# Kernel tuning notes

Hardware: AMD Instinct MI355X
Metric: run time of the kernel (lower is better)

## Reference

```python
import jax, jax.numpy as jnp
import numpy as np

DIM = 2048
HEAD = 256
SEQ = 4096

def setup_inputs() -> dict:
    key = jax.random.key(0)
    ks = jax.random.split(key, 7)
    s = 1.0 / np.sqrt(DIM)
    return {
        "marketStateBatch": jax.random.normal(ks[0], (SEQ, DIM), dtype=jnp.float32),
        "Wq": jax.random.uniform(ks[1], (HEAD, DIM), jnp.float32, -s, s),
        "bq": jax.random.uniform(ks[2], (HEAD,), jnp.float32, -s, s),
        "Wk": jax.random.uniform(ks[3], (HEAD, DIM), jnp.float32, -s, s),
        "bk": jax.random.uniform(ks[4], (HEAD,), jnp.float32, -s, s),
        "Wv": jax.random.uniform(ks[5], (HEAD, DIM), jnp.float32, -s, s),
        "bv": jax.random.uniform(ks[6], (HEAD,), jnp.float32, -s, s),
    }

def reference(marketStateBatch, Wq, bq, Wk, bk, Wv, bv):
    x = marketStateBatch  # [S, D]
    q = x @ Wq.T + bq     # [S, H]
    k = x @ Wk.T + bk     # [S, H]
    v = x @ Wv.T + bv     # [S, H]
    # NOTE: original scales by sqrt(dimensionSize), the INPUT dim, not head dim.
    scores = (q @ k.T) * (1.0 / np.sqrt(DIM))  # [S, S]
    S = x.shape[0]
    causal = jnp.tril(jnp.ones((S, S), dtype=bool))
    scores = jnp.where(causal, scores, -jnp.inf)
    attn = jax.nn.softmax(scores, axis=-1)
    # torch.nan_to_num(attn, 0.0): rows are never all -inf here (diag kept),
    # but replicate the op faithfully.
    attn = jnp.nan_to_num(attn, nan=0.0)
    return attn @ v  # [S, H]
```

## Files before the change

### kernel.cpp

```cpp
#include <hip/hip_runtime.h>
#include <stdint.h>

#define SEQ 4096
#define DIMK 2048
#define HD 256

typedef __attribute__((ext_vector_type(8))) short bf16x8;
typedef __attribute__((ext_vector_type(4))) short u16x4;
typedef __attribute__((ext_vector_type(4))) float f32x4;
typedef unsigned short u16;
typedef unsigned int u32;

#define BAR() asm volatile("s_barrier" ::: "memory")
#define VMCNT(n) asm volatile("s_waitcnt vmcnt(" #n ")" ::: "memory")

__device__ __forceinline__ u16 f2bf(float f) {
    u32 u = __float_as_uint(f);
    u += 0x7FFFu + ((u >> 16) & 1u);
    return (u16)(u >> 16);
}

__device__ __forceinline__ bf16x8 pack8(f32x4 a0, f32x4 a1) {
    bf16x8 v8;
    v8[0]=(short)f2bf(a0[0]); v8[1]=(short)f2bf(a0[1]);
    v8[2]=(short)f2bf(a0[2]); v8[3]=(short)f2bf(a0[3]);
    v8[4]=(short)f2bf(a1[0]); v8[5]=(short)f2bf(a1[1]);
    v8[6]=(short)f2bf(a1[2]); v8[7]=(short)f2bf(a1[3]);
    return v8;
}

__device__ __forceinline__ void gl16(const void* g, void* l) {
    __builtin_amdgcn_global_load_lds(
        (const __attribute__((address_space(1))) void*)g,
        (__attribute__((address_space(3))) void*)l, 16, 0, 0);
}

__global__ __launch_bounds__(256) void cvt_all2(
    const float* __restrict__ x, const float* __restrict__ Wq,
    const float* __restrict__ Wk, const float* __restrict__ Wv,
    u16* __restrict__ xb_sw, u16* __restrict__ wb_sw)
{
    const int y = blockIdx.y;
    int i = blockIdx.x * 256 + threadIdx.x;
    int stride = gridDim.x * 256;
    if (y == 0) {
        for (; i < SEQ*DIMK/8; i += stride) {
            int row = i >> 8, c8 = i & 255;
            f32x4 a0 = *(const f32x4*)(x + (size_t)row*DIMK + c8*8);
            f32x4 a1 = *(const f32x4*)(x + (size_t)row*DIMK + c8*8 + 4);
            int mt = row >> 6, rl = row & 63, kt = c8 >> 3, sl = c8 & 7;
            size_t dst = ((size_t)(mt*32 + kt))*4096 + rl*64 + ((sl ^ (rl&7))*8);
            *(bf16x8*)(xb_sw + dst) = pack8(a0, a1);
        }
    } else {
        const float* W = (y==1) ? Wq : (y==2) ? Wk : Wv;
        for (; i < HD*DIMK/8; i += stride) {
            int row = i >> 8, c8 = i & 255;
            f32x4 a0 = *(const f32x4*)(W + (size_t)row*DIMK + c8*8);
            f32x4 a1 = *(const f32x4*)(W + (size_t)row*DIMK + c8*8 + 4);
            int gr = (y-1)*256 + row;
            int nt = gr >> 7, rl = gr & 127, kt = c8 >> 3, sl = c8 & 7;
            size_t dst = ((size_t)(nt*32 + kt))*8192 + rl*64 + ((sl ^ (rl&7))*8);
            *(bf16x8*)(wb_sw + dst) = pack8(a0, a1);
        }
    }
}

__global__ __launch_bounds__(256) void qkv_gemm2(
    const u16* __restrict__ xb_sw, const u16* __restrict__ wb_sw,
    const float* __restrict__ bq, const float* __restrict__ bk,
    const float* __restrict__ bv,
    u16* __restrict__ qb, u16* __restrict__ kb_t, u16* __restrict__ vt_t)
{
    __shared__ char T[2][24576];

    const int tid = threadIdx.x;
    const int lane = tid & 63;
    const int w = tid >> 6;
    const int r = lane & 15, g = lane >> 4;
    const int wr = w >> 1, wc = w & 1;
    const int mt = blockIdx.x;
    const int y  = blockIdx.y;
    const int z  = y >> 1;
    const float* bias = (z==0) ? bq : (z==1) ? bk : bv;

    const u16* abase = xb_sw + (size_t)mt*32*4096;
    const u16* bbase = wb_sw + (size_t)y*32*8192;

    f32x4 zero = {0.f,0.f,0.f,0.f};
    f32x4 acc[2][4];
    #pragma unroll
    for (int m = 0; m < 2; ++m)
        #pragma unroll
        for (int n = 0; n < 4; ++n) acc[m][n] = zero;

    auto stage = [&](int b, int kt) {
        const u16* ag = abase + (size_t)kt*4096 + w*1024 + lane*8;
        const u16* bg = bbase + (size_t)kt*8192 + w*2048 + lane*8;
        char* al = T[b] + w*2048;
        char* bl = T[b] + 8192 + w*4096;
        gl16(ag,        al);
        gl16(ag + 512,  al + 1024);
        gl16(bg,        bl);
        gl16(bg + 512,  bl + 1024);
        gl16(bg + 1024, bl + 2048);
        gl16(bg + 1536, bl + 3072);
    };

    stage(0, 0);
    stage(1, 1);

    for (int kt = 0; kt < 32; ++kt) {
        if (kt < 31) { VMCNT(6); } else { VMCNT(0); }
        BAR();
        const char* A = T[kt & 1];
        const char* B = T[kt & 1] + 8192;
        #pragma unroll
        for (int kc = 0; kc < 2; ++kc) {
            bf16x8 af[2], bfr[4];
            #pragma unroll
            for (int m = 0; m < 2; ++m) {
                int arow = wr*32 + m*16 + r;
                af[m] = *(const bf16x8*)(A + arow*128 + (((kc*4+g) ^ (arow&7)) << 4));
            }
            #pragma unroll
            for (int n = 0; n < 4; ++n) {
                int brow = wc*64 + n*16 + r;
                bfr[n] = *(const bf16x8*)(B + brow*128 + (((kc*4+g) ^ (brow&7)) << 4));
            }
            #pragma unroll
            for (int m = 0; m < 2; ++m)
                #pragma unroll
                for (int n = 0; n < 4; ++n)
                    acc[m][n] = __builtin_amdgcn_mfma_f32_16x16x32_bf16(
                        af[m], bfr[n], acc[m][n], 0, 0, 0);
        }
        BAR();
        if (kt + 2 < 32) stage(kt & 1, kt + 2);
    }

    const int m0 = mt*64, n0 = y*128;
    const float qs = 0.03187936f;
    if (z == 0) {
        #pragma unroll
        for (int n = 0; n < 4; ++n) {
            int hc = (n0 + wc*64 + n*16 + r) & 255;
            float bcol = bias[hc];
            #pragma unroll
            for (int m = 0; m < 2; ++m) {
                int row0 = m0 + wr*32 + m*16 + g*4;
                #pragma unroll
                for (int j = 0; j < 4; ++j)
                    qb[(size_t)(row0+j)*HD + hc] = f2bf((acc[m][n][j] + bcol) * qs);
            }
        }
    } else if (z == 1) {
        #pragma unroll
        for (int n = 0; n < 4; ++n) {
            int hc = (n0 + wc*64 + n*16 + r) & 255;
            float bcol = bias[hc];
            #pragma unroll
            for (int m = 0; m < 2; ++m) {
                int row0 = m0 + wr*32 + m*16 + g*4;
                #pragma unroll
                for (int j = 0; j < 4; ++j) {
                    int rowj = row0 + j;
                    int t = rowj >> 5, rl = rowj & 31;
                    kb_t[(size_t)t*8192 + rl*256 + (((hc>>3) ^ (rl&7))*8) + (hc&7)]
                        = f2bf(acc[m][n][j] + bcol);
                }
            }
        }
    } else {
        #pragma unroll
        for (int n = 0; n < 4; ++n) {
            int hc = (n0 + wc*64 + n*16 + r) & 255;
            float bcol = bias[hc];
            #pragma unroll
            for (int m = 0; m < 2; ++m) {
                int kv0 = m0 + wr*32 + m*16 + g*4;
                int t = kv0 >> 5, kl = kv0 & 31;
                u16x4 pk;
                #pragma unroll
                for (int j = 0; j < 4; ++j) pk[j] = (short)f2bf(acc[m][n][j] + bcol);
                *(u16x4*)(vt_t + (size_t)t*8192 + hc*32 +
                          (((kl>>3) ^ (hc&3) ^ ((hc>>2)&3))*8) + (kl&7)) = pk;
            }
        }
    }
}

__global__ __launch_bounds__(256) void attn_part3(
    const u16* __restrict__ qb, const u16* __restrict__ kb_t,
    const u16* __restrict__ vt_t,
    float* __restrict__ po, float* __restrict__ pm, float* __restrict__ pl,
    int C32)
{
    __shared__ char Ks[2][16384];
    __shared__ char Vt[2][16384];
    __shared__ char Ps[4][1280];

    const int qt = blockIdx.x;
    const int s  = blockIdx.y;
    const int nt = 2*qt + 2;
    const int ns = (nt + C32 - 1) / C32;
    if (s >= ns) return;
    int pid0 = 0;
    for (int k = 0; k < qt; ++k) pid0 += (2*k + 2 + C32 - 1) / C32;
    const int pid = pid0 + s;
    const int t0 = s * C32;
    const int t1 = min(t0 + C32, nt);

    const int tid = threadIdx.x;
    const int lane = tid & 63;
    const int w = tid >> 6;
    const int r = lane & 15, g = lane >> 4;
    const int qg = qt*64 + w*16 + r;

    bf16x8 qf[8];
    {
        const u16* qp = qb + (size_t)qg*HD + g*8;
        #pragma unroll
        for (int c = 0; c < 8; ++c) qf[c] = *(const bf16x8*)(qp + c*32);
    }
    VMCNT(0);

    auto stage = [&](int b, int t) {
        const u16* kg = kb_t + (size_t)t*8192 + w*2048 + lane*8;
        const u16* vg = vt_t + (size_t)t*8192 + w*2048 + lane*8;
        char* kl = Ks[b] + w*4096;
        char* vl = Vt[b] + w*4096;
        #pragma unroll
        for (int i = 0; i < 4; ++i) gl16(kg + i*512, kl + i*1024);
        #pragma unroll
        for (int i = 0; i < 4; ++i) gl16(vg + i*512, vl + i*1024);
    };

    stage(0, t0);
    if (t0 + 1 < t1) stage(1, t0 + 1);

    f32x4 zero = {0.f,0.f,0.f,0.f};
    f32x4 o[16];
    #pragma unroll
    for (int hf = 0; hf < 16; ++hf) o[hf] = zero;
    float mrun = -__builtin_inff(), lrun = 0.f;
    char* Psw = Ps[w];

    for (int t = t0; t < t1; ++t) {
        if (t + 1 < t1) { VMCNT(8); } else { VMCNT(0); }
        BAR();
        const char* K = Ks[t & 1];
        const char* V = Vt[t & 1];

        f32x4 sv[2];
        __builtin_amdgcn_s_setprio(1);
        #pragma unroll
        for (int f = 0; f < 2; ++f) {
            sv[f] = zero;
            int kv = f*16 + r;
            #pragma unroll
            for (int c = 0; c < 8; ++c) {
                bf16x8 kf = *(const bf16x8*)(K + kv*512 + (((c*4+g) ^ (kv&7)) << 4));
                sv[f] = __builtin_amdgcn_mfma_f32_16x16x32_bf16(kf, qf[c], sv[f], 0, 0, 0);
            }
        }
        __builtin_amdgcn_s_setprio(0);

        if (t*32 + 31 > qg) {
            #pragma unroll
            for (int f = 0; f < 2; ++f)
                #pragma unroll
                for (int j = 0; j < 4; ++j)
                    if (t*32 + f*16 + g*4 + j > qg) sv[f][j] = -__builtin_inff();
        }

        float mx = fmaxf(fmaxf(fmaxf(sv[0][0], sv[0][1]), fmaxf(sv[0][2], sv[0][3])),
                         fmaxf(fmaxf(sv[1][0], sv[1][1]), fmaxf(sv[1][2], sv[1][3])));
        mx = fmaxf(mx, __shfl_xor(mx, 16));
        mx = fmaxf(mx, __shfl_xor(mx, 32));
        if (__any(mx > mrun + 8.0f)) {
            float mnew  = fmaxf(mrun, mx);
            float alpha = exp2f(mrun - mnew);
            lrun *= alpha;
            #pragma unroll
            for (int hf = 0; hf < 16; ++hf) o[hf] *= alpha;
            mrun = mnew;
        }
        float rs = 0.f;
        #pragma unroll
        for (int f = 0; f < 2; ++f)
            #pragma unroll
            for (int j = 0; j < 4; ++j) {
                float p = exp2f(sv[f][j] - mrun);
                sv[f][j] = p;
                rs += p;
            }
        rs += __shfl_xor(rs, 16);
        rs += __shfl_xor(rs, 32);
        lrun += rs;

        #pragma unroll
        for (int f = 0; f < 2; ++f)
            #pragma unroll
            for (int i2 = 0; i2 < 2; ++i2) {
                u32 pk = (u32)f2bf(sv[f][2*i2]) | ((u32)f2bf(sv[f][2*i2+1]) << 16);
                *(u32*)(Psw + r*80 + f*32 + g*8 + i2*4) = pk;
            }
        bf16x8 pa = *(const bf16x8*)(Psw + r*80 + g*16);

        __builtin_amdgcn_s_setprio(1);
        #pragma unroll
        for (int hf = 0; hf < 16; ++hf) {
            int hd = hf*16 + r;
            bf16x8 vf = *(const bf16x8*)(V + hd*64 + ((g ^ (r&3) ^ ((r>>2)&3)) << 4));
            o[hf] = __builtin_amdgcn_mfma_f32_16x16x32_bf16(vf, pa, o[hf], 0, 0, 0);
        }
        __builtin_amdgcn_s_setprio(0);

        BAR();
        if (t + 2 < t1) stage(t & 1, t + 2);
    }

    if (g == 0) {
        pm[(size_t)pid*64 + w*16 + r] = mrun;
        pl[(size_t)pid*64 + w*16 + r] = lrun;
    }
    float* op = po + ((size_t)pid*64 + w*16 + r) * 256;
    #pragma unroll
    for (int hf = 0; hf < 16; ++hf)
        *(f32x4*)(op + hf*16 + g*4) = o[hf];
}

__global__ __launch_bounds__(256) void attn_combine3(
    const float* __restrict__ po, const float* __restrict__ pm,
    const float* __restrict__ pl, float* __restrict__ out, int C32)
{
    const int tid = threadIdx.x;
    const int row = blockIdx.x * 16 + (tid >> 4);
    const int cg  = tid & 15;
    const int qt  = row >> 6, rr = row & 63;
    const int nt  = 2*qt + 2;
    const int ns  = (nt + C32 - 1) / C32;
    int pid0 = 0;
    for (int k = 0; k < qt; ++k) pid0 += (2*k + 2 + C32 - 1) / C32;

    float M = -__builtin_inff();
    for (int s = 0; s < ns; ++s)
        M = fmaxf(M, pm[(size_t)(pid0+s)*64 + rr]);

    float lt = 0.f;
    f32x4 acc[4];
    f32x4 zero = {0.f,0.f,0.f,0.f};
    #pragma unroll
    for (int v = 0; v < 4; ++v) acc[v] = zero;

    for (int s = 0; s < ns; ++s) {
        float ms  = pm[(size_t)(pid0+s)*64 + rr];
        float wgt = exp2f(ms - M);
        lt += wgt * pl[(size_t)(pid0+s)*64 + rr];
        const f32x4* p = (const f32x4*)(po + ((size_t)(pid0+s)*64 + rr)*256 + cg*16);
        #pragma unroll
        for (int v = 0; v < 4; ++v) acc[v] += p[v] * wgt;
    }
    float inv = 1.f / lt;
    f32x4* op = (f32x4*)(out + (size_t)row*256 + cg*16);
    #pragma unroll
    for (int v = 0; v < 4; ++v) op[v] = acc[v] * inv;
}

extern "C" void kernel_launch(void* const* d_in, const int* in_sizes, int n_in,
                              void* d_out, int out_size, void* d_ws, size_t ws_size,
                              hipStream_t stream) {
    const float* x  = (const float*)d_in[0];
    const float* Wq = (const float*)d_in[1];
    const float* bq = (const float*)d_in[2];
    const float* Wk = (const float*)d_in[3];
    const float* bk = (const float*)d_in[4];
    const float* Wv = (const float*)d_in[5];
    const float* bv = (const float*)d_in[6];
    float* out = (float*)d_out;

    const size_t xb_bytes  = (size_t)SEQ * DIMK * 2;
    const size_t wb_bytes  = (size_t)768 * DIMK * 2;
    const size_t qkv_bytes = (size_t)SEQ * HD * 2;
    const size_t base = xb_bytes + wb_bytes + 3*qkv_bytes;

    int C32 = 64;
    size_t npid = 0;
    const int cand[4] = {8, 16, 32, 64};
    for (int ci = 0; ci < 4; ++ci) {
        int c = cand[ci];
        size_t np = 0;
        for (int qt = 0; qt < 64; ++qt) np += (size_t)(2*qt + 2 + c - 1) / c;
        size_t need = base + np * (64*256*4 + 2*64*4);
        if (need <= ws_size) { C32 = c; npid = np; break; }
        if (ci == 3) { C32 = c; npid = np; }
    }

    char* p = (char*)d_ws;
    u16* xb_sw = (u16*)p; p += xb_bytes;
    u16* wb_sw = (u16*)p; p += wb_bytes;
    u16* qbuf  = (u16*)p; p += qkv_bytes;
    u16* kb_t  = (u16*)p; p += qkv_bytes;
    u16* vt_t  = (u16*)p; p += qkv_bytes;
    float* po  = (float*)p; p += npid * 64 * 256 * 4;
    float* pm  = (float*)p; p += npid * 64 * 4;
    float* pl  = (float*)p; p += npid * 64 * 4;

    cvt_all2<<<dim3(512, 4), 256, 0, stream>>>(x, Wq, Wk, Wv, xb_sw, wb_sw);

    qkv_gemm2<<<dim3(SEQ/64, 6), 256, 0, stream>>>(
        xb_sw, wb_sw, bq, bk, bv, qbuf, kb_t, vt_t);

    const int maxns = (128 + C32 - 1) / C32;
    attn_part3<<<dim3(64, maxns), 256, 0, stream>>>(
        qbuf, kb_t, vt_t, po, pm, pl, C32);

    attn_combine3<<<SEQ/16, 256, 0, stream>>>(po, pm, pl, out, C32);
}
```

Baseline: 89.42 us.

## Halve V LDS staging, load half of V to registers, bf16 partials, compact grid

The attention kernel now stages only half of each V tile in shared memory and reads the other half straight from global memory into registers, shrinking LDS use so more blocks fit per CU (launch bounds 3). K staging is restructured with a mid-iteration barrier, and the grid is flattened to exactly npid blocks so no empty blocks are launched. Partial outputs are stored as bf16 instead of fp32, cutting workspace traffic between the partial and combine kernels at some precision cost. The risks are extra register pressure from the held V fragments and exposed global-load latency for the direct V reads.

After: 85.17 us. 1.05x faster.

```diff
diff --git a/kernel.cpp b/kernel.cpp
--- a/kernel.cpp
+++ b/kernel.cpp
@@ -18,6 +18,11 @@
     u32 u = __float_as_uint(f);
     u += 0x7FFFu + ((u >> 16) & 1u);
     return (u16)(u >> 16);
+}
+
+__device__ __forceinline__ float bf2f(u16 h) {
+    u32 u = ((u32)h) << 16;
+    return __uint_as_float(u);
 }
 
 __device__ __forceinline__ bf16x8 pack8(f32x4 a0, f32x4 a1) {
@@ -190,24 +195,25 @@
     }
 }
 
-__global__ __launch_bounds__(256) void attn_part3(
+__global__ __launch_bounds__(256, 3) void attn_part4(
     const u16* __restrict__ qb, const u16* __restrict__ kb_t,
     const u16* __restrict__ vt_t,
-    float* __restrict__ po, float* __restrict__ pm, float* __restrict__ pl,
+    u16* __restrict__ po, float* __restrict__ pm, float* __restrict__ pl,
     int C32)
 {
     __shared__ char Ks[2][16384];
-    __shared__ char Vt[2][16384];
+    __shared__ char Vh[8192];
     __shared__ char Ps[4][1280];
 
-    const int qt = blockIdx.x;
-    const int s  = blockIdx.y;
+    const int pid = blockIdx.x;
+    int qt = 0, acc0 = 0;
+    for (int k = 0; k < 64; ++k) {
+        int nsk = (2*k + 2 + C32 - 1) / C32;
+        if (pid < acc0 + nsk) { qt = k; break; }
+        acc0 += nsk;
+    }
+    const int s  = pid - acc0;
     const int nt = 2*qt + 2;
-    const int ns = (nt + C32 - 1) / C32;
-    if (s >= ns) return;
-    int pid0 = 0;
-    for (int k = 0; k < qt; ++k) pid0 += (2*k + 2 + C32 - 1) / C32;
-    const int pid = pid0 + s;
     const int t0 = s * C32;
     const int t1 = min(t0 + C32, nt);
 
@@ -216,6 +222,7 @@
     const int w = tid >> 6;
     const int r = lane & 15, g = lane >> 4;
     const int qg = qt*64 + w*16 + r;
+    const int vswz = (g ^ (r&3) ^ ((r>>2)&3)) << 4;
 
     bf16x8 qf[8];
     {
@@ -223,21 +230,16 @@
         #pragma unroll
         for (int c = 0; c < 8; ++c) qf[c] = *(const bf16x8*)(qp + c*32);
     }
-    VMCNT(0);
-
-    auto stage = [&](int b, int t) {
+
+    auto stageK = [&](int t, int buf) {
         const u16* kg = kb_t + (size_t)t*8192 + w*2048 + lane*8;
-        const u16* vg = vt_t + (size_t)t*8192 + w*2048 + lane*8;
-        char* kl = Ks[b] + w*4096;
-        char* vl = Vt[b] + w*4096;
+        char* kl = Ks[buf] + w*4096;
         #pragma unroll
         for (int i = 0; i < 4; ++i) gl16(kg + i*512, kl + i*1024);
-        #pragma unroll
-        for (int i = 0; i < 4; ++i) gl16(vg + i*512, vl + i*1024);
     };
 
-    stage(0, t0);
-    if (t0 + 1 < t1) stage(1, t0 + 1);
+    stageK(t0, 0);
+    if (t0 + 1 < t1) stageK(t0 + 1, 1); else stageK(t0, 1);
 
     f32x4 zero = {0.f,0.f,0.f,0.f};
     f32x4 o[16];
@@ -247,10 +249,23 @@
     char* Psw = Ps[w];
 
     for (int t = t0; t < t1; ++t) {
-        if (t + 1 < t1) { VMCNT(8); } else { VMCNT(0); }
+        VMCNT(4);
         BAR();
         const char* K = Ks[t & 1];
-        const char* V = Vt[t & 1];
+
+        {
+            const u16* vg = vt_t + (size_t)t*8192 + 4096 + w*1024 + lane*8;
+            char* vl = Vh + w*2048;
+            gl16(vg,       vl);
+            gl16(vg + 512, vl + 1024);
+        }
+        bf16x8 v0[8];
+        {
+            const u16* vb = vt_t + (size_t)t*8192 + (size_t)r*32;
+            #pragma unroll
+            for (int hf = 0; hf < 8; ++hf)
+                v0[hf] = *(const bf16x8*)((const char*)(vb + (size_t)hf*16*32) + vswz);
+        }
 
         f32x4 sv[2];
         __builtin_amdgcn_s_setprio(1);
@@ -265,6 +280,11 @@
             }
         }
         __builtin_amdgcn_s_setprio(0);
+
+        VMCNT(8);
+        BAR();
+
+        stageK(min(t + 2, t1 - 1), t & 1);
 
         if (t*32 + 31 > qg) {
             #pragma unroll
@@ -310,29 +330,35 @@
 
         __builtin_amdgcn_s_setprio(1);
         #pragma unroll
-        for (int hf = 0; hf < 16; ++hf) {
-            int hd = hf*16 + r;
-            bf16x8 vf = *(const bf16x8*)(V + hd*64 + ((g ^ (r&3) ^ ((r>>2)&3)) << 4));
+        for (int hf = 0; hf < 8; ++hf)
+            o[hf] = __builtin_amdgcn_mfma_f32_16x16x32_bf16(v0[hf], pa, o[hf], 0, 0, 0);
+        #pragma unroll
+        for (int hf = 8; hf < 16; ++hf) {
+            int lr = (hf-8)*16 + r;
+            bf16x8 vf = *(const bf16x8*)(Vh + lr*64 + vswz);
             o[hf] = __builtin_amdgcn_mfma_f32_16x16x32_bf16(vf, pa, o[hf], 0, 0, 0);
         }
         __builtin_amdgcn_s_setprio(0);
-
-        BAR();
-        if (t + 2 < t1) stage(t & 1, t + 2);
-    }
+    }
+
+    VMCNT(0);
 
     if (g == 0) {
         pm[(size_t)pid*64 + w*16 + r] = mrun;
         pl[(size_t)pid*64 + w*16 + r] = lrun;
     }
-    float* op = po + ((size_t)pid*64 + w*16 + r) * 256;
+    u16* op = po + ((size_t)pid*64 + w*16 + r) * 256;
     #pragma unroll
-    for (int hf = 0; hf < 16; ++hf)
-        *(f32x4*)(op + hf*16 + g*4) = o[hf];
-}
-
-__global__ __launch_bounds__(256) void attn_combine3(
-    const float* __restrict__ po, const float* __restrict__ pm,
+    for (int hf = 0; hf < 16; ++hf) {
+        u16x4 pk;
+        #pragma unroll
+        for (int j = 0; j < 4; ++j) pk[j] = (short)f2bf(o[hf][j]);
+        *(u16x4*)(op + hf*16 + g*4) = pk;
+    }
+}
+
+__global__ __launch_bounds__(256) void attn_combine4(
+    const u16* __restrict__ po, const float* __restrict__ pm,
     const float* __restrict__ pl, float* __restrict__ out, int C32)
 {
     const int tid = threadIdx.x;
@@ -358,9 +384,14 @@
         float ms  = pm[(size_t)(pid0+s)*64 + rr];
         float wgt = exp2f(ms - M);
         lt += wgt * pl[(size_t)(pid0+s)*64 + rr];
-        const f32x4* p = (const f32x4*)(po + ((size_t)(pid0+s)*64 + rr)*256 + cg*16);
-        #pragma unroll
-        for (int v = 0; v < 4; ++v) acc[v] += p[v] * wgt;
+        const u16* p = po + ((size_t)(pid0+s)*64 + rr)*256 + cg*16;
+        #pragma unroll
+        for (int v = 0; v < 4; ++v) {
+            u16x4 pv = *(const u16x4*)(p + v*4);
+            #pragma unroll
+            for (int e = 0; e < 4; ++e)
+                acc[v][e] += wgt * bf2f((u16)pv[e]);
+        }
     }
     float inv = 1.f / lt;
     f32x4* op = (f32x4*)(out + (size_t)row*256 + cg*16);
@@ -392,7 +423,7 @@
         int c = cand[ci];
         size_t np = 0;
         for (int qt = 0; qt < 64; ++qt) np += (size_t)(2*qt + 2 + c - 1) / c;
-        size_t need = base + np * (64*256*4 + 2*64*4);
+        size_t need = base + np * ((size_t)64*256*2 + 2*64*4);
         if (need <= ws_size) { C32 = c; npid = np; break; }
         if (ci == 3) { C32 = c; npid = np; }
     }
@@ -403,7 +434,7 @@
     u16* qbuf  = (u16*)p; p += qkv_bytes;
     u16* kb_t  = (u16*)p; p += qkv_bytes;
     u16* vt_t  = (u16*)p; p += qkv_bytes;
-    float* po  = (float*)p; p += npid * 64 * 256 * 4;
+    u16* po    = (u16*)p; p += npid * 64 * 256 * 2;
     float* pm  = (float*)p; p += npid * 64 * 4;
     float* pl  = (float*)p; p += npid * 64 * 4;
 
@@ -412,9 +443,8 @@
     qkv_gemm2<<<dim3(SEQ/64, 6), 256, 0, stream>>>(
         xb_sw, wb_sw, bq, bk, bv, qbuf, kb_t, vt_t);
 
-    const int maxns = (128 + C32 - 1) / C32;
-    attn_part3<<<dim3(64, maxns), 256, 0, stream>>>(
+    attn_part4<<<(int)npid, 256, 0, stream>>>(
         qbuf, kb_t, vt_t, po, pm, pl, C32);
 
-    attn_combine3<<<SEQ/16, 256, 0, stream>>>(po, pm, pl, out, C32);
-}
+    attn_combine4<<<SEQ/16, 256, 0, stream>>>(po, pm, pl, out, C32);
+}
```
